# Kernel tuning notes

Hardware: AMD Instinct MI355X
Metric: run time of the kernel (lower is better)

The kernel has to match this reference:

```python
import jax, jax.numpy as jnp
import numpy as np

B, S, D = 2, 2048, 1024
H = 16
HD = D // H
MAXPOS = 2048


def setup_inputs() -> dict:
    key = jax.random.key(0)
    ks = jax.random.split(key, 10)
    sc = 1.0 / np.sqrt(D)
    inp = {
        "x": jax.random.normal(ks[0], (B, S, D), dtype=jnp.float32),
        "Wq": jax.random.normal(ks[1], (D, D), dtype=jnp.float32) * sc,
        "bq": jnp.zeros((D,), dtype=jnp.float32),
        "Wk": jax.random.normal(ks[2], (D, D), dtype=jnp.float32) * sc,
        "bk": jnp.zeros((D,), dtype=jnp.float32),
        "Wv": jax.random.normal(ks[3], (D, D), dtype=jnp.float32) * sc,
        "bv": jnp.zeros((D,), dtype=jnp.float32),
        "Wo": jax.random.normal(ks[4], (D, D), dtype=jnp.float32) * sc,
        "bo": jnp.zeros((D,), dtype=jnp.float32),
        "rel_bias": jax.random.normal(ks[5], (2 * MAXPOS - 1, H), dtype=jnp.float32) * 0.02,
    }
    return inp


def reference(x, Wq, bq, Wk, bk, Wv, bv, Wo, bo, rel_bias):
    b, s, _ = x.shape
    # QKV projections (torch Linear: x @ W.T + b)
    Q = (x @ Wq.T + bq).reshape(b, s, H, HD).transpose(0, 2, 1, 3)  # [b,h,s,hd]
    K = (x @ Wk.T + bk).reshape(b, s, H, HD).transpose(0, 2, 1, 3)
    V = (x @ Wv.T + bv).reshape(b, s, H, HD).transpose(0, 2, 1, 3)

    content_scores = jnp.einsum("bhqd,bhkd->bhqk", Q, K)

    # relative position index: q_ids - k_ids + (key_len - 1), sliced to seq
    q_ids = jnp.arange(s)[:, None]
    k_ids = jnp.arange(s)[None, :]
    rel_idx = q_ids - k_ids + (MAXPOS - 1)  # [s,s], values in [0, 2*MAXPOS-2]
    bias = rel_bias[rel_idx]  # [s,s,h]
    bias = jnp.transpose(bias, (2, 0, 1))  # [h,s,s]

    scores = (content_scores + bias[None]) / np.sqrt(HD)
    weights = jax.nn.softmax(scores, axis=-1)  # [b,h,s,s]

    out = jnp.einsum("bhqk,bhkd->bhqd", weights, V)
    out = out.transpose(0, 2, 1, 3).reshape(b, s, D)
    out = out @ Wo.T + bo
    return out, weights
```

## Files before the change

kernel.cpp:

```cpp
#include <hip/hip_runtime.h>
#include <cstdint>
#include <cstddef>

typedef unsigned short u16;
typedef __attribute__((ext_vector_type(4)))  u16    u16x4;
typedef __attribute__((ext_vector_type(8)))  u16    u16x8;
typedef __attribute__((ext_vector_type(8)))  __bf16 bf16x8;
typedef __attribute__((ext_vector_type(4)))  float  f32x4;
typedef __attribute__((ext_vector_type(16))) float  f32x16;

#define BB 2
#define SS 2048
#define DD 1024
#define HH 16
#define HDD 64

__device__ __forceinline__ u16 f2bf(float f) {
  unsigned u = __builtin_bit_cast(unsigned, f);
  u += 0x7FFFu + ((u >> 16) & 1u);
  return (u16)(u >> 16);
}

__device__ __forceinline__ f32x16 mfma32(u16x8 a, u16x8 b, f32x16 c) {
  return __builtin_amdgcn_mfma_f32_32x32x16_bf16(
      __builtin_bit_cast(bf16x8, a), __builtin_bit_cast(bf16x8, b), c, 0, 0, 0);
}
__device__ __forceinline__ f32x4 mfma16(u16x8 a, u16x8 b, f32x4 c) {
  return __builtin_amdgcn_mfma_f32_16x16x32_bf16(
      __builtin_bit_cast(bf16x8, a), __builtin_bit_cast(bf16x8, b), c, 0, 0, 0);
}

__device__ __forceinline__ void gload16(const u16* g, u16* l) {
  typedef const __attribute__((address_space(1))) unsigned GQ;
  typedef __attribute__((address_space(3))) unsigned LQ;
  __builtin_amdgcn_global_load_lds((GQ*)(uintptr_t)g, (LQ*)(uint32_t)(uintptr_t)l,
                                   16, 0, 0);
}

__global__ __launch_bounds__(256) void mhsa_convert(
    const float* __restrict__ x, const float* __restrict__ wq,
    const float* __restrict__ wk, const float* __restrict__ wv,
    const float* __restrict__ wo,
    u16* __restrict__ xb, u16* __restrict__ wpack, u16* __restrict__ wob) {
  const size_t NX = (size_t)BB * SS * DD;
  const size_t NW = (size_t)DD * DD;
  const size_t nch = (NX + 4 * NW) >> 2;
  for (size_t i = (size_t)blockIdx.x * 256 + threadIdx.x; i < nch;
       i += (size_t)gridDim.x * 256) {
    size_t e = i << 2;
    const float* s; u16* d;
    if (e < NX)               { s = x  + e;                d = xb + e; }
    else if (e < NX + NW)     { s = wq + (e - NX);         d = wpack + (e - NX); }
    else if (e < NX + 2 * NW) { s = wk + (e - NX - NW);    d = wpack + (e - NX); }
    else if (e < NX + 3 * NW) { s = wv + (e - NX - 2*NW);  d = wpack + (e - NX); }
    else                      { s = wo + (e - NX - 3*NW);  d = wob + (e - NX - 3*NW); }
    f32x4 v = *(const f32x4*)s;
    u16x4 o; o[0] = f2bf(v[0]); o[1] = f2bf(v[1]); o[2] = f2bf(v[2]); o[3] = f2bf(v[3]);
    *(u16x4*)d = o;
  }
}

__global__ __launch_bounds__(256) void mhsa_gemm_qkv(
    const u16* __restrict__ A, const u16* __restrict__ Bm,
    const float* __restrict__ bq, const float* __restrict__ bk,
    const float* __restrict__ bv,
    u16* __restrict__ Q, u16* __restrict__ K, u16* __restrict__ V) {
  const int KD = DD;
  __shared__ __attribute__((aligned(16))) u16 lA[128 * 64];
  __shared__ __attribute__((aligned(16))) u16 lB[128 * 64];
  int tid = threadIdx.x;
  int bm = blockIdx.y, bn = blockIdx.x;
  int l = tid & 63, w = tid >> 6, wr = w >> 1, wc = w & 1;
  int l15 = l & 15, l4 = l >> 4;
  f32x4 acc[4][4];
#pragma unroll
  for (int mi = 0; mi < 4; mi++)
#pragma unroll
    for (int ni = 0; ni < 4; ni++)
#pragma unroll
      for (int j = 0; j < 4; j++) acc[mi][ni][j] = 0.f;

  const u16* Ag = A + (size_t)bm * 128 * KD;
  const u16* Bg = Bm + (size_t)bn * 128 * KD;
  const int srow = (l >> 3), scol = (l & 7) * 8;
  for (int kt = 0; kt < KD / 64; kt++) {
    const u16* As = Ag + (size_t)(w * 32 + srow) * KD + kt * 64 + scol;
    const u16* Bs = Bg + (size_t)(w * 32 + srow) * KD + kt * 64 + scol;
    u16* Ad = &lA[(w * 32) * 64];
    u16* Bd = &lB[(w * 32) * 64];
#pragma unroll
    for (int t = 0; t < 4; t++) {
      gload16(As + (size_t)t * 8 * KD, Ad + t * 8 * 64);
      gload16(Bs + (size_t)t * 8 * KD, Bd + t * 8 * 64);
    }
    __syncthreads();
#pragma unroll
    for (int kk = 0; kk < 64; kk += 32) {
      u16x8 af[4], bf[4];
#pragma unroll
      for (int mi = 0; mi < 4; mi++)
        af[mi] = *(const u16x8*)&lA[(wr * 64 + mi * 16 + l15) * 64 + kk + l4 * 8];
#pragma unroll
      for (int ni = 0; ni < 4; ni++)
        bf[ni] = *(const u16x8*)&lB[(wc * 64 + ni * 16 + l15) * 64 + kk + l4 * 8];
#pragma unroll
      for (int mi = 0; mi < 4; mi++)
#pragma unroll
        for (int ni = 0; ni < 4; ni++)
          acc[mi][ni] = mfma16(af[mi], bf[ni], acc[mi][ni]);
    }
    __syncthreads();
  }
  int rowbase = bm * 128 + wr * 64;
  int colbase = bn * 128 + wc * 64;
#pragma unroll
  for (int ni = 0; ni < 4; ni++) {
    int col = colbase + ni * 16 + l15;
    int which = col >> 10, cc = col & 1023;
    const float* bp = (which == 0) ? bq : (which == 1) ? bk : bv;
    u16* dst = (which == 0) ? Q : (which == 1) ? K : V;
    float bias = bp[cc];
    int h = cc >> 6, hd = cc & 63;
#pragma unroll
    for (int mi = 0; mi < 4; mi++) {
#pragma unroll
      for (int j = 0; j < 4; j++) {
        int row = rowbase + mi * 16 + l4 * 4 + j;
        int b = row >> 11, s = row & 2047;
        dst[(((size_t)b * HH + h) * SS + s) * HDD + hd] = f2bf(acc[mi][ni][j] + bias);
      }
    }
  }
}

__global__ __launch_bounds__(256) void mhsa_transpose_v(
    const u16* __restrict__ Vb, u16* __restrict__ Vt) {
  __shared__ u16 t[64][72];
  int st = blockIdx.x, bh = blockIdx.y;
  int tid = threadIdx.x;
  int r = tid >> 2, c0 = (tid & 3) * 16;
  const u16* src = Vb + ((size_t)bh * SS + st * 64) * HDD;
  u16x8 v0 = *(const u16x8*)&src[r * 64 + c0];
  u16x8 v1 = *(const u16x8*)&src[r * 64 + c0 + 8];
#pragma unroll
  for (int j = 0; j < 8; j++) { t[r][c0 + j] = v0[j]; t[r][c0 + 8 + j] = v1[j]; }
  __syncthreads();
  u16* dst = Vt + ((size_t)bh * HDD + r) * SS + st * 64 + c0;
  u16x8 o0, o1;
#pragma unroll
  for (int j = 0; j < 8; j++) { o0[j] = t[c0 + j][r]; o1[j] = t[c0 + 8 + j][r]; }
  *(u16x8*)&dst[0] = o0;
  *(u16x8*)&dst[8] = o1;
}

__global__ __launch_bounds__(512, 2) void mhsa_attn(
    const u16* __restrict__ Qb, const u16* __restrict__ Kb,
    const u16* __restrict__ Vt, const float* __restrict__ rel_bias,
    float* __restrict__ wout, u16* __restrict__ attn) {
  int qb = blockIdx.x, bh = blockIdx.y;
  int h = bh & (HH - 1);
  int q0 = qb * 32;
  int tid = threadIdx.x;
  int w = tid >> 6, l = tid & 63, l31 = l & 31, hi = l >> 5;

  __shared__ float bias_lds[2080];
  __shared__ float red[8][32];
  __shared__ float gval[32];
  __shared__ __attribute__((aligned(16))) u16 plds[8][32][40];
  __shared__ float pvred[4][32][64];

  for (int i = tid; i < 2079; i += 512)
    bias_lds[i] = rel_bias[(size_t)(q0 + i) * HH + h];

  const u16* Qp = Qb + ((size_t)bh * SS + q0) * HDD;
  u16x8 aq[4];
#pragma unroll
  for (int c = 0; c < 4; c++)
    aq[c] = *(const u16x8*)&Qp[l31 * 64 + c * 16 + hi * 8];

  __syncthreads();

  int rowq[16];
#pragma unroll
  for (int r = 0; r < 16; r++) rowq[r] = (r & 3) + 8 * (r >> 2) + 4 * hi;

  const u16* Kp = Kb + (size_t)bh * SS * HDD;
  f32x16 acc[8];
  float s16[16];
#pragma unroll
  for (int r = 0; r < 16; r++) s16[r] = 0.f;
#pragma unroll
  for (int kt = 0; kt < 8; kt++) {
    int kg = w * 256 + kt * 32;
    f32x16 a;
#pragma unroll
    for (int j = 0; j < 16; j++) a[j] = 0.f;
#pragma unroll
    for (int c = 0; c < 4; c++) {
      u16x8 kf = *(const u16x8*)&Kp[(size_t)(kg + l31) * 64 + c * 16 + hi * 8];
      a = mfma32(aq[c], kf, a);
    }
    int kgl = kg + l31;
#pragma unroll
    for (int r = 0; r < 16; r++) {
      float sc = (a[r] + bias_lds[rowq[r] + 2047 - kgl]) * 0.125f;
      float p = exp2f(sc * 1.4426950408889634f);
      a[r] = p;
      s16[r] += p;
    }
    acc[kt] = a;
  }
#pragma unroll
  for (int mask = 1; mask <= 16; mask <<= 1)
#pragma unroll
    for (int r = 0; r < 16; r++) s16[r] += __shfl_xor(s16[r], mask);
  if (l31 == 0) {
#pragma unroll
    for (int r = 0; r < 16; r++) red[w][rowq[r]] = s16[r];
  }
  __syncthreads();
  if (tid < 32) {
    float g = 0.f;
#pragma unroll
    for (int ww = 0; ww < 8; ww++) g += red[ww][tid];
    gval[tid] = g;
  }
  __syncthreads();
  float inv16[16];
#pragma unroll
  for (int r = 0; r < 16; r++) inv16[r] = 1.0f / gval[rowq[r]];

  float* wbase = wout + ((size_t)bh * SS + q0) * (size_t)SS;
  const u16* Vp = Vt + (size_t)bh * HDD * SS;
  f32x16 pv0, pv1;
#pragma unroll
  for (int j = 0; j < 16; j++) { pv0[j] = 0.f; pv1[j] = 0.f; }

#pragma unroll
  for (int kt = 0; kt < 8; kt++) {
    int kg = w * 256 + kt * 32;
#pragma unroll
    for (int r = 0; r < 16; r++) {
      float wv = acc[kt][r] * inv16[r];
      acc[kt][r] = wv;
      __builtin_nontemporal_store(wv, &wbase[(size_t)rowq[r] * SS + kg + l31]);
    }
#pragma unroll
    for (int r = 0; r < 16; r++)
      plds[w][rowq[r]][l31] = f2bf(acc[kt][r]);
#pragma unroll
    for (int kk = 0; kk < 32; kk += 16) {
      u16x8 pa  = *(const u16x8*)&plds[w][l31][kk + hi * 8];
      u16x8 vb0 = *(const u16x8*)&Vp[(size_t)l31 * SS + kg + kk + hi * 8];
      u16x8 vb1 = *(const u16x8*)&Vp[(size_t)(32 + l31) * SS + kg + kk + hi * 8];
      pv0 = mfma32(pa, vb0, pv0);
      pv1 = mfma32(pa, vb1, pv1);
    }
  }
  if (w >= 4) {
#pragma unroll
    for (int r = 0; r < 16; r++) {
      pvred[w - 4][rowq[r]][l31]      = pv0[r];
      pvred[w - 4][rowq[r]][32 + l31] = pv1[r];
    }
  }
  __syncthreads();
  if (w < 4) {
#pragma unroll
    for (int r = 0; r < 16; r++) {
      pvred[w][rowq[r]][l31]      += pv0[r];
      pvred[w][rowq[r]][32 + l31] += pv1[r];
    }
  }
  __syncthreads();
  int b = bh >> 4;
  for (int idx = tid; idx < 2048; idx += 512) {
    int qq = idx >> 6, hd = idx & 63;
    float sum = 0.f;
#pragma unroll
    for (int ww = 0; ww < 4; ww++) sum += pvred[ww][qq][hd];
    attn[((size_t)b * SS + q0 + qq) * DD + h * HDD + hd] = f2bf(sum);
  }
}

__global__ __launch_bounds__(256) void mhsa_gemm_out(
    const u16* __restrict__ A, const u16* __restrict__ Bm,
    const float* __restrict__ bo, float* __restrict__ out) {
  const int KD = DD;
  __shared__ __attribute__((aligned(16))) u16 lA[128 * 64];
  __shared__ __attribute__((aligned(16))) u16 lB[64 * 64];
  int tid = threadIdx.x;
  int bm = blockIdx.y, bn = blockIdx.x;
  int l = tid & 63, w = tid >> 6, wr = w >> 1, wc = w & 1;
  int l15 = l & 15, l4 = l >> 4;
  f32x4 acc[4][2];
#pragma unroll
  for (int mi = 0; mi < 4; mi++)
#pragma unroll
    for (int ni = 0; ni < 2; ni++)
#pragma unroll
      for (int j = 0; j < 4; j++) acc[mi][ni][j] = 0.f;

  const u16* Ag = A + (size_t)bm * 128 * KD;
  const u16* Bg = Bm + (size_t)bn * 64 * KD;
  const int srow = (l >> 3), scol = (l & 7) * 8;
  for (int kt = 0; kt < KD / 64; kt++) {
    const u16* As = Ag + (size_t)(w * 32 + srow) * KD + kt * 64 + scol;
    const u16* Bs = Bg + (size_t)(w * 16 + srow) * KD + kt * 64 + scol;
    u16* Ad = &lA[(w * 32) * 64];
    u16* Bd = &lB[(w * 16) * 64];
#pragma unroll
    for (int t = 0; t < 4; t++)
      gload16(As + (size_t)t * 8 * KD, Ad + t * 8 * 64);
#pragma unroll
    for (int t = 0; t < 2; t++)
      gload16(Bs + (size_t)t * 8 * KD, Bd + t * 8 * 64);
    __syncthreads();
#pragma unroll
    for (int kk = 0; kk < 64; kk += 32) {
      u16x8 af[4], bf[2];
#pragma unroll
      for (int mi = 0; mi < 4; mi++)
        af[mi] = *(const u16x8*)&lA[(wr * 64 + mi * 16 + l15) * 64 + kk + l4 * 8];
#pragma unroll
      for (int ni = 0; ni < 2; ni++)
        bf[ni] = *(const u16x8*)&lB[(wc * 32 + ni * 16 + l15) * 64 + kk + l4 * 8];
#pragma unroll
      for (int mi = 0; mi < 4; mi++)
#pragma unroll
        for (int ni = 0; ni < 2; ni++)
          acc[mi][ni] = mfma16(af[mi], bf[ni], acc[mi][ni]);
    }
    __syncthreads();
  }
  int rowbase = bm * 128 + wr * 64;
  int colbase = bn * 64 + wc * 32;
#pragma unroll
  for (int ni = 0; ni < 2; ni++) {
    int col = colbase + ni * 16 + l15;
    float bias = bo[col];
#pragma unroll
    for (int mi = 0; mi < 4; mi++) {
#pragma unroll
      for (int j = 0; j < 4; j++) {
        int row = rowbase + mi * 16 + l4 * 4 + j;
        out[(size_t)row * DD + col] = acc[mi][ni][j] + bias;
      }
    }
  }
}

extern "C" void kernel_launch(void* const* d_in, const int* in_sizes, int n_in,
                              void* d_out, int out_size, void* d_ws, size_t ws_size,
                              hipStream_t stream) {
  const float* x  = (const float*)d_in[0];
  const float* Wq = (const float*)d_in[1];
  const float* bq = (const float*)d_in[2];
  const float* Wk = (const float*)d_in[3];
  const float* bk = (const float*)d_in[4];
  const float* Wv = (const float*)d_in[5];
  const float* bv = (const float*)d_in[6];
  const float* Wo = (const float*)d_in[7];
  const float* bo = (const float*)d_in[8];
  const float* rb = (const float*)d_in[9];

  char* ws = (char*)d_ws;
  u16* xb    = (u16*)(ws + 0);
  u16* wpack = (u16*)(ws + 8388608);
  u16* wob   = (u16*)(ws + 14680064);
  u16* Qb    = (u16*)(ws + 16777216);
  u16* Kb    = (u16*)(ws + 25165824);
  u16* Vb    = (u16*)(ws + 33554432);
  u16* Vt    = (u16*)(ws + 41943040);
  u16* attnb = (u16*)(ws + 50331648);
  if (ws_size < 58720256) return;

  float* out   = (float*)d_out;
  float* wout  = out + (size_t)BB * SS * DD;

  mhsa_convert<<<2048, 256, 0, stream>>>(x, Wq, Wk, Wv, Wo, xb, wpack, wob);
  mhsa_gemm_qkv<<<dim3(24, 32), 256, 0, stream>>>(xb, wpack, bq, bk, bv, Qb, Kb, Vb);
  mhsa_transpose_v<<<dim3(32, 32), 256, 0, stream>>>(Vb, Vt);
  mhsa_attn<<<dim3(64, 32), 512, 0, stream>>>(Qb, Kb, Vt, rb, wout, attnb);
  mhsa_gemm_out<<<dim3(16, 32), 256, 0, stream>>>(attnb, wob, bo, out);
}
```

Baseline: 281.1 us.

## Fuse V transpose into QKV GEMM epilogue and prefold softmax scale into Q

The QKV GEMM epilogue now writes V directly in transposed [b,h,hd,s] layout, which removes the separate transpose kernel launch and the round trip of V through global memory. It also folds the 1/sqrt(HD)*log2(e) factor into Q at projection time and into the staged relative bias, so the attention inner loop needs a single add before exp2. Rounding Q to bf16 after scaling changes numerics slightly, and the transposed V stores are 8-byte scattered writes.

```diff
diff --git a/kernel.cpp b/kernel.cpp
--- a/kernel.cpp
+++ b/kernel.cpp
@@ -14,6 +14,7 @@
 #define DD 1024
 #define HH 16
 #define HDD 64
+#define QSCL 0.18033688011112042f
 
 __device__ __forceinline__ u16 f2bf(float f) {
   unsigned u = __builtin_bit_cast(unsigned, f);
@@ -64,7 +65,7 @@
     const u16* __restrict__ A, const u16* __restrict__ Bm,
     const float* __restrict__ bq, const float* __restrict__ bk,
     const float* __restrict__ bv,
-    u16* __restrict__ Q, u16* __restrict__ K, u16* __restrict__ V) {
+    u16* __restrict__ Q, u16* __restrict__ K, u16* __restrict__ Vt) {
   const int KD = DD;
   __shared__ __attribute__((aligned(16))) u16 lA[128 * 64];
   __shared__ __attribute__((aligned(16))) u16 lB[128 * 64];
@@ -118,39 +119,33 @@
     int col = colbase + ni * 16 + l15;
     int which = col >> 10, cc = col & 1023;
     const float* bp = (which == 0) ? bq : (which == 1) ? bk : bv;
-    u16* dst = (which == 0) ? Q : (which == 1) ? K : V;
     float bias = bp[cc];
+    float scl = (which == 0) ? QSCL : 1.0f;
     int h = cc >> 6, hd = cc & 63;
-#pragma unroll
-    for (int mi = 0; mi < 4; mi++) {
-#pragma unroll
-      for (int j = 0; j < 4; j++) {
-        int row = rowbase + mi * 16 + l4 * 4 + j;
-        int b = row >> 11, s = row & 2047;
-        dst[(((size_t)b * HH + h) * SS + s) * HDD + hd] = f2bf(acc[mi][ni][j] + bias);
+    if (which < 2) {
+      u16* dst = (which == 0) ? Q : K;
+#pragma unroll
+      for (int mi = 0; mi < 4; mi++) {
+#pragma unroll
+        for (int j = 0; j < 4; j++) {
+          int row = rowbase + mi * 16 + l4 * 4 + j;
+          int b = row >> 11, s = row & 2047;
+          dst[(((size_t)b * HH + h) * SS + s) * HDD + hd] =
+              f2bf((acc[mi][ni][j] + bias) * scl);
+        }
       }
-    }
-  }
-}
-
-__global__ __launch_bounds__(256) void mhsa_transpose_v(
-    const u16* __restrict__ Vb, u16* __restrict__ Vt) {
-  __shared__ u16 t[64][72];
-  int st = blockIdx.x, bh = blockIdx.y;
-  int tid = threadIdx.x;
-  int r = tid >> 2, c0 = (tid & 3) * 16;
-  const u16* src = Vb + ((size_t)bh * SS + st * 64) * HDD;
-  u16x8 v0 = *(const u16x8*)&src[r * 64 + c0];
-  u16x8 v1 = *(const u16x8*)&src[r * 64 + c0 + 8];
-#pragma unroll
-  for (int j = 0; j < 8; j++) { t[r][c0 + j] = v0[j]; t[r][c0 + 8 + j] = v1[j]; }
-  __syncthreads();
-  u16* dst = Vt + ((size_t)bh * HDD + r) * SS + st * 64 + c0;
-  u16x8 o0, o1;
-#pragma unroll
-  for (int j = 0; j < 8; j++) { o0[j] = t[c0 + j][r]; o1[j] = t[c0 + 8 + j][r]; }
-  *(u16x8*)&dst[0] = o0;
-  *(u16x8*)&dst[8] = o1;
+    } else {
+#pragma unroll
+      for (int mi = 0; mi < 4; mi++) {
+        int s0 = rowbase + mi * 16 + l4 * 4;
+        int b = s0 >> 11, s = s0 & 2047;
+        u16x4 o;
+#pragma unroll
+        for (int j = 0; j < 4; j++) o[j] = f2bf(acc[mi][ni][j] + bias);
+        *(u16x4*)&Vt[(((size_t)b * HH + h) * HDD + hd) * SS + s] = o;
+      }
+    }
+  }
 }
 
 __global__ __launch_bounds__(512, 2) void mhsa_attn(
@@ -170,7 +165,7 @@
   __shared__ float pvred[4][32][64];
 
   for (int i = tid; i < 2079; i += 512)
-    bias_lds[i] = rel_bias[(size_t)(q0 + i) * HH + h];
+    bias_lds[i] = rel_bias[(size_t)(q0 + i) * HH + h] * QSCL;
 
   const u16* Qp = Qb + ((size_t)bh * SS + q0) * HDD;
   u16x8 aq[4];
@@ -203,8 +198,7 @@
     int kgl = kg + l31;
 #pragma unroll
     for (int r = 0; r < 16; r++) {
-      float sc = (a[r] + bias_lds[rowq[r] + 2047 - kgl]) * 0.125f;
-      float p = exp2f(sc * 1.4426950408889634f);
+      float p = exp2f(a[r] + bias_lds[rowq[r] + 2047 - kgl]);
       a[r] = p;
       s16[r] += p;
     }
@@ -370,17 +364,15 @@
   u16* wob   = (u16*)(ws + 14680064);
   u16* Qb    = (u16*)(ws + 16777216);
   u16* Kb    = (u16*)(ws + 25165824);
-  u16* Vb    = (u16*)(ws + 33554432);
-  u16* Vt    = (u16*)(ws + 41943040);
-  u16* attnb = (u16*)(ws + 50331648);
-  if (ws_size < 58720256) return;
+  u16* Vt    = (u16*)(ws + 33554432);
+  u16* attnb = (u16*)(ws + 41943040);
+  if (ws_size < 50331648) return;
 
   float* out   = (float*)d_out;
   float* wout  = out + (size_t)BB * SS * DD;
 
   mhsa_convert<<<2048, 256, 0, stream>>>(x, Wq, Wk, Wv, Wo, xb, wpack, wob);
-  mhsa_gemm_qkv<<<dim3(24, 32), 256, 0, stream>>>(xb, wpack, bq, bk, bv, Qb, Kb, Vb);
-  mhsa_transpose_v<<<dim3(32, 32), 256, 0, stream>>>(Vb, Vt);
+  mhsa_gemm_qkv<<<dim3(24, 32), 256, 0, stream>>>(xb, wpack, bq, bk, bv, Qb, Kb, Vt);
   mhsa_attn<<<dim3(64, 32), 512, 0, stream>>>(Qb, Kb, Vt, rb, wout, attnb);
   mhsa_gemm_out<<<dim3(16, 32), 256, 0, stream>>>(attnb, wob, bo, out);
 }
```

Measured after the change: 288.0 us. 1.02x slower.

## Stage QKV epilogue through LDS for vectorized stores; prefold softmax scale into Q

Applied to the files above, without the earlier changes.

The QKV GEMM epilogue now writes the tile into padded shared memory and then emits 16-byte vector stores to the head-major Q/K/V layout, replacing scattered 2-byte stores. The 1/sqrt(hd)*log2(e) factor is folded into Q at projection time and into the relative bias when loaded, so the attention inner loop drops two multiplies per score. This adds an extra LDS pass and a barrier in the epilogue. Rounding Q to bf16 after scaling changes numerics slightly.

```diff
diff --git a/kernel.cpp b/kernel.cpp
--- a/kernel.cpp
+++ b/kernel.cpp
@@ -14,6 +14,7 @@
 #define DD 1024
 #define HH 16
 #define HDD 64
+#define QSCL 0.18033688011112042f
 
 __device__ __forceinline__ u16 f2bf(float f) {
   unsigned u = __builtin_bit_cast(unsigned, f);
@@ -66,8 +67,9 @@
     const float* __restrict__ bv,
     u16* __restrict__ Q, u16* __restrict__ K, u16* __restrict__ V) {
   const int KD = DD;
-  __shared__ __attribute__((aligned(16))) u16 lA[128 * 64];
-  __shared__ __attribute__((aligned(16))) u16 lB[128 * 64];
+  __shared__ __attribute__((aligned(16))) u16 smem[128 * 136];
+  u16* lA = smem;
+  u16* lB = smem + 8192;
   int tid = threadIdx.x;
   int bm = blockIdx.y, bn = blockIdx.x;
   int l = tid & 63, w = tid >> 6, wr = w >> 1, wc = w & 1;
@@ -111,25 +113,35 @@
     }
     __syncthreads();
   }
-  int rowbase = bm * 128 + wr * 64;
-  int colbase = bn * 128 + wc * 64;
+  const int which = (bn * 128) >> 10;
+  const float* bp = (which == 0) ? bq : (which == 1) ? bk : bv;
+  u16* dst = (which == 0) ? Q : (which == 1) ? K : V;
+  const float scl = (which == 0) ? QSCL : 1.0f;
 #pragma unroll
   for (int ni = 0; ni < 4; ni++) {
-    int col = colbase + ni * 16 + l15;
-    int which = col >> 10, cc = col & 1023;
-    const float* bp = (which == 0) ? bq : (which == 1) ? bk : bv;
-    u16* dst = (which == 0) ? Q : (which == 1) ? K : V;
-    float bias = bp[cc];
+    int col = bn * 128 + wc * 64 + ni * 16 + l15;
+    float bias = bp[col & 1023];
+    int lc = wc * 64 + ni * 16 + l15;
+#pragma unroll
+    for (int mi = 0; mi < 4; mi++) {
+#pragma unroll
+      for (int j = 0; j < 4; j++) {
+        int lr = wr * 64 + mi * 16 + l4 * 4 + j;
+        smem[lr * 136 + lc] = f2bf((acc[mi][ni][j] + bias) * scl);
+      }
+    }
+  }
+  __syncthreads();
+#pragma unroll
+  for (int t = 0; t < 8; t++) {
+    int idx = tid + t * 256;
+    int row = idx >> 4, c8 = idx & 15;
+    u16x8 v = *(const u16x8*)&smem[row * 136 + c8 * 8];
+    int sg = bm * 128 + row;
+    int b = sg >> 11, s = sg & 2047;
+    int cc = (bn * 128 + c8 * 8) & 1023;
     int h = cc >> 6, hd = cc & 63;
-#pragma unroll
-    for (int mi = 0; mi < 4; mi++) {
-#pragma unroll
-      for (int j = 0; j < 4; j++) {
-        int row = rowbase + mi * 16 + l4 * 4 + j;
-        int b = row >> 11, s = row & 2047;
-        dst[(((size_t)b * HH + h) * SS + s) * HDD + hd] = f2bf(acc[mi][ni][j] + bias);
-      }
-    }
+    *(u16x8*)&dst[(((size_t)b * HH + h) * SS + s) * HDD + hd] = v;
   }
 }
 
@@ -170,7 +182,7 @@
   __shared__ float pvred[4][32][64];
 
   for (int i = tid; i < 2079; i += 512)
-    bias_lds[i] = rel_bias[(size_t)(q0 + i) * HH + h];
+    bias_lds[i] = rel_bias[(size_t)(q0 + i) * HH + h] * QSCL;
 
   const u16* Qp = Qb + ((size_t)bh * SS + q0) * HDD;
   u16x8 aq[4];
@@ -203,8 +215,7 @@
     int kgl = kg + l31;
 #pragma unroll
     for (int r = 0; r < 16; r++) {
-      float sc = (a[r] + bias_lds[rowq[r] + 2047 - kgl]) * 0.125f;
-      float p = exp2f(sc * 1.4426950408889634f);
+      float p = exp2f(a[r] + bias_lds[rowq[r] + 2047 - kgl]);
       a[r] = p;
       s16[r] += p;
     }
```

New measurement: 277.0 us, median of 2. No clear change (-1.5%).
